# Optimization experiments

Measured on AMD Instinct MI355X. Metric: run time of the kernel, lower is better.

Reference implementation:

```python
import jax, jax.numpy as jnp
import numpy as np

NUM_CLASS = 4
SZ, SA = 3, 5            # LCN_HEIGHT, LCN_WIDTH
PZ, PA = SZ // 2, SA // 2  # 'same' padding (1, 2)
ANG_THETA_SQ = 0.9 ** 2
BI_THETA_SQ = 0.9 ** 2
ANG_COEF = 0.02
BI_COEF = 0.1
ITERS = 3


def _gauss_kernel(theta_sq):
    # angular_filter_kernel: Gaussian over spatial offsets, center zeroed
    dz = np.arange(SZ) - SZ // 2
    da = np.arange(SA) - SA // 2
    d2 = dz[:, None] ** 2 + da[None, :] ** 2
    k = np.exp(-d2 / (2.0 * theta_sq))
    k[SZ // 2, SA // 2] = 0.0
    return jnp.asarray(k, jnp.float32)


def _depthwise(x, k2d):
    # per-class diagonal conv (kernel identical across classes)
    w = jnp.tile(k2d[None, None], (NUM_CLASS, 1, 1, 1))  # [C,1,SZ,SA]
    return jax.lax.conv_general_dilated(
        x, w, window_strides=(1, 1), padding=[(PZ, PZ), (PA, PA)],
        feature_group_count=NUM_CLASS,
        dimension_numbers=('NCHW', 'OIHW', 'NCHW'))


def _neighbor_stack(x):
    # condensing_kernel conv: gather the 14 non-center neighbors per pixel
    B, C, H, W = x.shape
    p = jnp.pad(x, ((0, 0), (0, 0), (PZ, PZ), (PA, PA)))
    slices = []
    for dz in range(SZ):
        for da in range(SA):
            if dz == SZ // 2 and da == SA // 2:
                continue
            slices.append(p[:, :, dz:dz + H, da:da + W])
    return jnp.stack(slices, axis=2)  # [B,C,14,H,W]


def _compat(y, coef):
    # 1x1 conv with (ones - I) * coef
    s = jnp.sum(y, axis=1, keepdims=True)
    return coef * (s - y)


def setup_inputs() -> dict:
    key = jax.random.key(0)
    k1, k2, k3 = jax.random.split(key, 3)
    x = jax.random.normal(k1, (32, NUM_CLASS, 64, 512), dtype=jnp.float32)
    lidar_mask = jnp.round(jax.random.uniform(k2, (32, 1, 64, 512), dtype=jnp.float32))
    bilateral_filters = jax.random.uniform(
        k3, (32, NUM_CLASS, SZ * SA - 1, 64, 512), dtype=jnp.float32)
    return {"x": x, "lidar_mask": lidar_mask, "bilateral_filters": bilateral_filters}


def reference(x, lidar_mask, bilateral_filters):
    ang_k = _gauss_kernel(ANG_THETA_SQ)
    bi_ang_k = _gauss_kernel(BI_THETA_SQ)
    out = x
    for _ in range(ITERS):
        unary = jax.nn.softmax(out, axis=-1)  # faithful to the port: softmax over azimuth
        ang = _depthwise(unary, ang_k)
        bi_ang = _depthwise(unary, bi_ang_k)
        stack = _neighbor_stack(unary * lidar_mask)        # [B,C,14,H,W]
        condensed = jnp.sum(stack * bilateral_filters, 2)  # [B,C,H,W]
        bi = condensed * lidar_mask * bi_ang
        pairwise = _compat(ang, ANG_COEF) + _compat(bi, BI_COEF)
        out = unary + pairwise
    return out
```

## Files before the change

kernel.cpp:

```cpp
#include <hip/hip_runtime.h>
#include <math.h>

#define BB 32
#define CC 4
#define HH 64
#define WW 512
#define HW (HH * WW)

__global__ __launch_bounds__(256) void softmax_rows(const float* __restrict__ in,
                                                    float* __restrict__ out) {
    const int gwave = (blockIdx.x * 256 + threadIdx.x) >> 6;
    const int lane  = threadIdx.x & 63;
    if (gwave >= BB * CC * HH) return;

    const float4* rowv = reinterpret_cast<const float4*>(in + (size_t)gwave * WW);
    float4* outv       = reinterpret_cast<float4*>(out + (size_t)gwave * WW);

    float4 a = rowv[lane];
    float4 b = rowv[lane + 64];

    float m = fmaxf(fmaxf(fmaxf(a.x, a.y), fmaxf(a.z, a.w)),
                    fmaxf(fmaxf(b.x, b.y), fmaxf(b.z, b.w)));
    #pragma unroll
    for (int off = 32; off; off >>= 1) m = fmaxf(m, __shfl_xor(m, off));

    a.x = expf(a.x - m); a.y = expf(a.y - m); a.z = expf(a.z - m); a.w = expf(a.w - m);
    b.x = expf(b.x - m); b.y = expf(b.y - m); b.z = expf(b.z - m); b.w = expf(b.w - m);

    float s = (a.x + a.y + a.z + a.w) + (b.x + b.y + b.z + b.w);
    #pragma unroll
    for (int off = 32; off; off >>= 1) s += __shfl_xor(s, off);

    const float inv = 1.0f / s;
    a.x *= inv; a.y *= inv; a.z *= inv; a.w *= inv;
    b.x *= inv; b.y *= inv; b.z *= inv; b.w *= inv;
    outv[lane]      = a;
    outv[lane + 64] = b;
}

__global__ __launch_bounds__(512) void crf_fused(const float* __restrict__ U,
                                                 const float* __restrict__ M,
                                                 const float* __restrict__ BF,
                                                 float* __restrict__ out,
                                                 float k1, float k2, float k4, float k5) {
    __shared__ float u_lds[CC][3][WW + 4];
    __shared__ float m_lds[3][WW + 4];

    const int bh = blockIdx.x;
    const int b  = bh >> 6;
    const int h  = bh & 63;
    const int t  = threadIdx.x;

    #pragma unroll
    for (int r = 0; r < 3; ++r) {
        const int hr = h + r - 1;
        const bool v = (hr >= 0) && (hr < HH);
        #pragma unroll
        for (int c = 0; c < CC; ++c)
            u_lds[c][r][2 + t] = v ? U[(((size_t)b * CC + c) * HH + hr) * WW + t] : 0.0f;
        m_lds[r][2 + t] = v ? M[((size_t)b * HH + hr) * WW + t] : 0.0f;
    }
    if (t < 2) {
        #pragma unroll
        for (int r = 0; r < 3; ++r) {
            #pragma unroll
            for (int c = 0; c < CC; ++c) {
                u_lds[c][r][t] = 0.0f;
                u_lds[c][r][WW + 2 + t] = 0.0f;
            }
            m_lds[r][t] = 0.0f;
            m_lds[r][WW + 2 + t] = 0.0f;
        }
    }
    __syncthreads();

    const int   rz[14] = {0,0,0,0,0, 1,1,1,1, 2,2,2,2,2};
    const int   ra[14] = {0,1,2,3,4, 0,1,3,4, 0,1,2,3,4};
    const float kw[14] = {k5,k2,k1,k2,k5, k4,k1,k1,k4, k5,k2,k1,k2,k5};

    const float mc = m_lds[1][2 + t];

    float ang[CC], bi[CC], uc[CC];
    #pragma unroll
    for (int c = 0; c < CC; ++c) {
        const float* bfp = BF + (((size_t)b * CC + c) * 14) * HW + (size_t)h * WW + t;
        float a = 0.0f, cd = 0.0f;
        #pragma unroll
        for (int n = 0; n < 14; ++n) {
            const float uv = u_lds[c][rz[n]][t + ra[n]];
            const float mv = m_lds[rz[n]][t + ra[n]];
            a = fmaf(kw[n], uv, a);
            cd = fmaf(bfp[(size_t)n * HW], uv * mv, cd);
        }
        ang[c] = a;
        bi[c]  = cd * mc * a;
        uc[c]  = u_lds[c][1][2 + t];
    }

    const float sa = ang[0] + ang[1] + ang[2] + ang[3];
    const float sb = bi[0] + bi[1] + bi[2] + bi[3];

    #pragma unroll
    for (int c = 0; c < CC; ++c) {
        const float pw = 0.02f * (sa - ang[c]) + 0.1f * (sb - bi[c]);
        out[(((size_t)b * CC + c) * HH + h) * WW + t] = uc[c] + pw;
    }
}

extern "C" void kernel_launch(void* const* d_in, const int* in_sizes, int n_in,
                              void* d_out, int out_size, void* d_ws, size_t ws_size,
                              hipStream_t stream) {
    const float* x    = (const float*)d_in[0];
    const float* mask = (const float*)d_in[1];
    const float* bf   = (const float*)d_in[2];
    float* out = (float*)d_out;
    float* U   = (float*)d_ws;

    const double ts2 = 2.0 * 0.9 * 0.9;
    const float k1 = (float)exp(-1.0 / ts2);
    const float k2 = (float)exp(-2.0 / ts2);
    const float k4 = (float)exp(-4.0 / ts2);
    const float k5 = (float)exp(-5.0 / ts2);

    const int rows = BB * CC * HH;
    const dim3 sgrid((rows + 3) / 4), sblk(256);
    const dim3 fgrid(BB * HH), fblk(512);

    softmax_rows<<<sgrid, sblk, 0, stream>>>(x, U);
    crf_fused<<<fgrid, fblk, 0, stream>>>(U, mask, bf, out, k1, k2, k4, k5);

    softmax_rows<<<sgrid, sblk, 0, stream>>>(out, U);
    crf_fused<<<fgrid, fblk, 0, stream>>>(U, mask, bf, out, k1, k2, k4, k5);

    softmax_rows<<<sgrid, sblk, 0, stream>>>(out, U);
    crf_fused<<<fgrid, fblk, 0, stream>>>(U, mask, bf, out, k1, k2, k4, k5);
}
```

Measured before the change: 440.0 us.

## Fuse softmax into CRF kernel epilogue and vectorize four pixels per thread

Each CRF block now computes the next iteration's row softmax directly from its output using block-wide reductions, writing to ping-pong workspace buffers, so two separate softmax launches and their intermediate global round trips are removed. Each thread now handles four adjacent pixels with float4 loads of the bilateral filters, mask and unary, and the same LDS window is reused across the four outputs. This trades a larger register footprint and 128-thread blocks (lower per-block parallelism) for fewer memory transactions and launches.

```diff
diff --git a/kernel.cpp b/kernel.cpp
--- a/kernel.cpp
+++ b/kernel.cpp
@@ -38,72 +38,161 @@
     outv[lane + 64] = b;
 }
 
-__global__ __launch_bounds__(512) void crf_fused(const float* __restrict__ U,
+__global__ __launch_bounds__(128) void crf_fused(const float* __restrict__ Uin,
                                                  const float* __restrict__ M,
                                                  const float* __restrict__ BF,
-                                                 float* __restrict__ out,
-                                                 float k1, float k2, float k4, float k5) {
-    __shared__ float u_lds[CC][3][WW + 4];
-    __shared__ float m_lds[3][WW + 4];
+                                                 float* __restrict__ Uout,
+                                                 float* __restrict__ Oout,
+                                                 const int final_iter,
+                                                 const float k1, const float k2,
+                                                 const float k4, const float k5) {
+    __shared__ float u_lds[CC][3][520];
+    __shared__ float m_lds[3][520];
+    __shared__ float red[2][CC];
 
     const int bh = blockIdx.x;
     const int b  = bh >> 6;
     const int h  = bh & 63;
     const int t  = threadIdx.x;
-
+    const int w0 = t << 2;
+
+    const float4 z4 = {0.f, 0.f, 0.f, 0.f};
     #pragma unroll
     for (int r = 0; r < 3; ++r) {
         const int hr = h + r - 1;
-        const bool v = (hr >= 0) && (hr < HH);
-        #pragma unroll
-        for (int c = 0; c < CC; ++c)
-            u_lds[c][r][2 + t] = v ? U[(((size_t)b * CC + c) * HH + hr) * WW + t] : 0.0f;
-        m_lds[r][2 + t] = v ? M[((size_t)b * HH + hr) * WW + t] : 0.0f;
-    }
-    if (t < 2) {
+        const bool v = (unsigned)hr < (unsigned)HH;
+        #pragma unroll
+        for (int c = 0; c < CC; ++c) {
+            float4 val = v ? *reinterpret_cast<const float4*>(
+                                 &Uin[(((size_t)b * CC + c) * HH + hr) * WW + w0]) : z4;
+            *reinterpret_cast<float4*>(&u_lds[c][r][4 + w0]) = val;
+        }
+        float4 mval = v ? *reinterpret_cast<const float4*>(
+                              &M[((size_t)b * HH + hr) * WW + w0]) : z4;
+        *reinterpret_cast<float4*>(&m_lds[r][4 + w0]) = mval;
+    }
+    if (t < 4) {
         #pragma unroll
         for (int r = 0; r < 3; ++r) {
             #pragma unroll
-            for (int c = 0; c < CC; ++c) {
-                u_lds[c][r][t] = 0.0f;
-                u_lds[c][r][WW + 2 + t] = 0.0f;
+            for (int c = 0; c < CC; ++c) { u_lds[c][r][t] = 0.f; u_lds[c][r][516 + t] = 0.f; }
+            m_lds[r][t] = 0.f; m_lds[r][516 + t] = 0.f;
+        }
+    }
+    __syncthreads();
+
+    float mwin[3][12];
+    #pragma unroll
+    for (int r = 0; r < 3; ++r)
+        #pragma unroll
+        for (int j = 0; j < 3; ++j)
+            *reinterpret_cast<float4*>(&mwin[r][4 * j]) =
+                *reinterpret_cast<const float4*>(&m_lds[r][w0 + 4 * j]);
+
+    const float kw_row[3][5] = {{k5, k2, k1, k2, k5},
+                                {k4, k1, 0.f, k1, k4},
+                                {k5, k2, k1, k2, k5}};
+
+    float ang[CC][4], bi[CC][4], uc[CC][4];
+    const float mc[4] = {mwin[1][4], mwin[1][5], mwin[1][6], mwin[1][7]};
+
+    #pragma unroll
+    for (int c = 0; c < CC; ++c) {
+        const float* bfp = BF + (((size_t)b * CC + c) * 14) * (size_t)HW + (size_t)h * WW + w0;
+        float a[4] = {0.f, 0.f, 0.f, 0.f}, d[4] = {0.f, 0.f, 0.f, 0.f};
+        int n = 0;
+        #pragma unroll
+        for (int r = 0; r < 3; ++r) {
+            float uwin[12];
+            #pragma unroll
+            for (int j = 0; j < 3; ++j)
+                *reinterpret_cast<float4*>(&uwin[4 * j]) =
+                    *reinterpret_cast<const float4*>(&u_lds[c][r][w0 + 4 * j]);
+            if (r == 1) {
+                uc[c][0] = uwin[4]; uc[c][1] = uwin[5];
+                uc[c][2] = uwin[6]; uc[c][3] = uwin[7];
             }
-            m_lds[r][t] = 0.0f;
-            m_lds[r][WW + 2 + t] = 0.0f;
-        }
-    }
-    __syncthreads();
-
-    const int   rz[14] = {0,0,0,0,0, 1,1,1,1, 2,2,2,2,2};
-    const int   ra[14] = {0,1,2,3,4, 0,1,3,4, 0,1,2,3,4};
-    const float kw[14] = {k5,k2,k1,k2,k5, k4,k1,k1,k4, k5,k2,k1,k2,k5};
-
-    const float mc = m_lds[1][2 + t];
-
-    float ang[CC], bi[CC], uc[CC];
-    #pragma unroll
-    for (int c = 0; c < CC; ++c) {
-        const float* bfp = BF + (((size_t)b * CC + c) * 14) * HW + (size_t)h * WW + t;
-        float a = 0.0f, cd = 0.0f;
-        #pragma unroll
-        for (int n = 0; n < 14; ++n) {
-            const float uv = u_lds[c][rz[n]][t + ra[n]];
-            const float mv = m_lds[rz[n]][t + ra[n]];
-            a = fmaf(kw[n], uv, a);
-            cd = fmaf(bfp[(size_t)n * HW], uv * mv, cd);
-        }
-        ang[c] = a;
-        bi[c]  = cd * mc * a;
-        uc[c]  = u_lds[c][1][2 + t];
-    }
-
-    const float sa = ang[0] + ang[1] + ang[2] + ang[3];
-    const float sb = bi[0] + bi[1] + bi[2] + bi[3];
-
-    #pragma unroll
-    for (int c = 0; c < CC; ++c) {
-        const float pw = 0.02f * (sa - ang[c]) + 0.1f * (sb - bi[c]);
-        out[(((size_t)b * CC + c) * HH + h) * WW + t] = uc[c] + pw;
+            #pragma unroll
+            for (int da = 0; da < 5; ++da) {
+                if (r == 1 && da == 2) continue;
+                const float kv = kw_row[r][da];
+                const float4 bfv = *reinterpret_cast<const float4*>(&bfp[(size_t)n * HW]);
+                const float bfa[4] = {bfv.x, bfv.y, bfv.z, bfv.w};
+                #pragma unroll
+                for (int q = 0; q < 4; ++q) {
+                    const float uv = uwin[q + da + 2];
+                    a[q] = fmaf(kv, uv, a[q]);
+                    d[q] = fmaf(bfa[q], uv * mwin[r][q + da + 2], d[q]);
+                }
+                ++n;
+            }
+        }
+        #pragma unroll
+        for (int q = 0; q < 4; ++q) {
+            ang[c][q] = a[q];
+            bi[c][q]  = d[q] * mc[q] * a[q];
+        }
+    }
+
+    float o[CC][4];
+    #pragma unroll
+    for (int q = 0; q < 4; ++q) {
+        const float sa = ang[0][q] + ang[1][q] + ang[2][q] + ang[3][q];
+        const float sb = bi[0][q] + bi[1][q] + bi[2][q] + bi[3][q];
+        #pragma unroll
+        for (int c = 0; c < CC; ++c)
+            o[c][q] = uc[c][q] + 0.02f * (sa - ang[c][q]) + 0.1f * (sb - bi[c][q]);
+    }
+
+    if (final_iter) {
+        #pragma unroll
+        for (int c = 0; c < CC; ++c) {
+            const float4 v = {o[c][0], o[c][1], o[c][2], o[c][3]};
+            *reinterpret_cast<float4*>(&Oout[(((size_t)b * CC + c) * HH + h) * WW + w0]) = v;
+        }
+        return;
+    }
+
+    const int lane = t & 63, wv = t >> 6;
+
+    float mx[CC];
+    #pragma unroll
+    for (int c = 0; c < CC; ++c) {
+        float v = fmaxf(fmaxf(o[c][0], o[c][1]), fmaxf(o[c][2], o[c][3]));
+        #pragma unroll
+        for (int off = 32; off; off >>= 1) v = fmaxf(v, __shfl_xor(v, off));
+        mx[c] = v;
+    }
+    if (lane == 0) {
+        #pragma unroll
+        for (int c = 0; c < CC; ++c) red[wv][c] = mx[c];
+    }
+    __syncthreads();
+    float gmx[CC];
+    #pragma unroll
+    for (int c = 0; c < CC; ++c) gmx[c] = fmaxf(red[0][c], red[1][c]);
+    __syncthreads();
+
+    float e[CC][4], sm[CC];
+    #pragma unroll
+    for (int c = 0; c < CC; ++c) {
+        float s = 0.f;
+        #pragma unroll
+        for (int q = 0; q < 4; ++q) { e[c][q] = expf(o[c][q] - gmx[c]); s += e[c][q]; }
+        #pragma unroll
+        for (int off = 32; off; off >>= 1) s += __shfl_xor(s, off);
+        sm[c] = s;
+    }
+    if (lane == 0) {
+        #pragma unroll
+        for (int c = 0; c < CC; ++c) red[wv][c] = sm[c];
+    }
+    __syncthreads();
+    #pragma unroll
+    for (int c = 0; c < CC; ++c) {
+        const float inv = 1.f / (red[0][c] + red[1][c]);
+        const float4 v = {e[c][0] * inv, e[c][1] * inv, e[c][2] * inv, e[c][3] * inv};
+        *reinterpret_cast<float4*>(&Uout[(((size_t)b * CC + c) * HH + h) * WW + w0]) = v;
     }
 }
 
@@ -114,7 +203,8 @@
     const float* mask = (const float*)d_in[1];
     const float* bf   = (const float*)d_in[2];
     float* out = (float*)d_out;
-    float* U   = (float*)d_ws;
+    float* U0  = (float*)d_ws;
+    float* U1  = U0 + (size_t)BB * CC * HH * WW;
 
     const double ts2 = 2.0 * 0.9 * 0.9;
     const float k1 = (float)exp(-1.0 / ts2);
@@ -122,16 +212,11 @@
     const float k4 = (float)exp(-4.0 / ts2);
     const float k5 = (float)exp(-5.0 / ts2);
 
-    const int rows = BB * CC * HH;
-    const dim3 sgrid((rows + 3) / 4), sblk(256);
-    const dim3 fgrid(BB * HH), fblk(512);
-
-    softmax_rows<<<sgrid, sblk, 0, stream>>>(x, U);
-    crf_fused<<<fgrid, fblk, 0, stream>>>(U, mask, bf, out, k1, k2, k4, k5);
-
-    softmax_rows<<<sgrid, sblk, 0, stream>>>(out, U);
-    crf_fused<<<fgrid, fblk, 0, stream>>>(U, mask, bf, out, k1, k2, k4, k5);
-
-    softmax_rows<<<sgrid, sblk, 0, stream>>>(out, U);
-    crf_fused<<<fgrid, fblk, 0, stream>>>(U, mask, bf, out, k1, k2, k4, k5);
+    const dim3 sgrid(2048), sblk(256);
+    const dim3 fgrid(BB * HH), fblk(128);
+
+    softmax_rows<<<sgrid, sblk, 0, stream>>>(x, U0);
+    crf_fused<<<fgrid, fblk, 0, stream>>>(U0, mask, bf, U1, out, 0, k1, k2, k4, k5);
+    crf_fused<<<fgrid, fblk, 0, stream>>>(U1, mask, bf, U0, out, 0, k1, k2, k4, k5);
+    crf_fused<<<fgrid, fblk, 0, stream>>>(U0, mask, bf, U0, out, 1, k1, k2, k4, k5);
 }
```

New measurement: 440.7 us. No clear change (+0.2%).
